# Kernel optimization log

Hardware: AMD Instinct MI355X
Metric: run time of the kernel (lower is better)

The kernel has to match this reference:

```python
import jax, jax.numpy as jnp
import numpy as np

BETA = 0.25  # VQ commitment cost


def setup_inputs() -> dict:
    key = jax.random.key(0)
    ks = jax.random.split(key, 6)
    B, C, H, W = 4096, 10, 32, 32
    Din, D, K = 3 * H * W, 256, 512
    img = jax.random.normal(ks[0], (B, 3, H, W), jnp.float32)
    label = jax.random.randint(ks[1], (B,), 0, C)
    enc_W = jax.random.normal(ks[2], (C, Din, D), jnp.float32) * (1.0 / np.sqrt(Din))
    enc_b = jnp.zeros((C, D), jnp.float32)
    codebook = jax.random.normal(ks[3], (K, D), jnp.float32)
    dec_W = jax.random.normal(ks[4], (D, Din), jnp.float32) * (1.0 / np.sqrt(D))
    dec_b = jnp.zeros((Din,), jnp.float32)
    return {"img": img, "label": label, "enc_W": enc_W, "enc_b": enc_b,
            "codebook": codebook, "dec_W": dec_W, "dec_b": dec_b}


def reference(img, label, enc_W, enc_b, codebook, dec_W, dec_b):
    B = img.shape[0]
    C = enc_W.shape[0]
    x = img.reshape(B, -1)                                   # [B, Din]
    onehot = jax.nn.one_hot(label, C, dtype=x.dtype)         # [B, C]
    # label-routed per-class encoders: encode with every expert, select by label
    z_all = jnp.einsum('bi,cid->bcd', x, enc_W) + enc_b[None]  # [B, C, D]
    z = jnp.einsum('bcd,bc->bd', z_all, onehot)              # [B, D]
    # --- VQ quantizer (shared) ---
    d2 = (jnp.sum(z * z, -1, keepdims=True)
          - 2.0 * (z @ codebook.T)
          + jnp.sum(codebook * codebook, -1)[None])          # [B, K]
    idx = jnp.argmin(d2, axis=-1)                            # [B]
    q = codebook[idx]                                        # [B, D]
    # per-sample VQ loss (mean over latent dim): codebook + beta*commitment
    cb_l = jnp.mean((jax.lax.stop_gradient(z) - q) ** 2, -1)
    cm_l = jnp.mean((z - jax.lax.stop_gradient(q)) ** 2, -1)
    l = cb_l + BETA * cm_l                                   # [B]
    q_st = z + jax.lax.stop_gradient(q - z)                  # straight-through
    # quantization loss = (sum over activated classes of per-subset mean) / n_activated
    counts = jax.ops.segment_sum(jnp.ones((B,), x.dtype), label, num_segments=C)
    sum_l = jax.ops.segment_sum(l, label, num_segments=C)
    present = counts > 0
    per_class = jnp.where(present, sum_l / jnp.maximum(counts, 1.0), 0.0)
    n_act = jnp.maximum(jnp.sum(present.astype(x.dtype)), 1.0)
    quant = jnp.sum(per_class) / n_act
    # shared decoder; scatter-back is identity here since every label has an expert
    dec = q_st @ dec_W + dec_b                               # [B, Din]
    img_out = dec.reshape(img.shape)
    loss = jnp.mean((img_out - img) ** 2) + quant
    return (loss, img_out)
```

## Files before the change

kernel.cpp:

```cpp
#include <hip/hip_runtime.h>
#include <hip/hip_bf16.h>
#include <stddef.h>

#define NB   4096
#define NC   10
#define DIN  3072
#define DD   256
#define KCB  512
#define KSPLIT 8
#define KC   (DIN / KSPLIT)
#define TM   64
#define TGRID 80
#define NIT  (KC / 32)

#define PW_C  786432
#define PW_NH 393216
#define PW_KS 49152
#define PW_IT 4096

typedef unsigned short u16;
typedef short s16x8 __attribute__((ext_vector_type(8)));
typedef float f32x4 __attribute__((ext_vector_type(4)));

__device__ inline void f2bf2(float f, u16& h, u16& l) {
    unsigned uf = __builtin_bit_cast(unsigned, f);
    unsigned uh = (uf + 0x7FFFu + ((uf >> 16) & 1u)) >> 16;
    h = (u16)uh;
    float fh = __builtin_bit_cast(float, uh << 16);
    float r = f - fh;
    unsigned ur = __builtin_bit_cast(unsigned, r);
    l = (u16)((ur + 0x7FFFu + ((ur >> 16) & 1u)) >> 16);
}

__global__ __launch_bounds__(256) void k_wtp(
    const int* __restrict__ label, const float* __restrict__ cb,
    const float* __restrict__ encW, const float* __restrict__ dW,
    int* __restrict__ meta, int* __restrict__ order, float* __restrict__ cbn,
    u16* __restrict__ WtH, u16* __restrict__ WtL,
    u16* __restrict__ dWtH, u16* __restrict__ dWtL, float* __restrict__ cbt)
{
    const int t = threadIdx.x;
    const int bid = blockIdx.x;
    if (bid == 0) {
        __shared__ int cnt_s[NC], cur_s[NC], off_s[NC];
        if (t < NC) { cnt_s[t] = 0; cur_s[t] = 0; }
        __syncthreads();
        for (int b = t; b < NB; b += 256) atomicAdd(&cnt_s[label[b]], 1);
        __syncthreads();
        if (t == 0) {
            int o = 0;
            for (int c = 0; c < NC; ++c) {
                off_s[c] = o; meta[c] = cnt_s[c]; meta[32 + c] = o; o += cnt_s[c];
            }
            meta[32 + NC] = o;
            int ntl = 0;
            for (int c = 0; c < NC; ++c)
                for (int r0 = 0; r0 < cnt_s[c]; r0 += TM) {
                    meta[64 + 2 * ntl] = c; meta[65 + 2 * ntl] = r0; ++ntl;
                }
            meta[63] = ntl;
        }
        __syncthreads();
        for (int b = t; b < NB; b += 256) {
            int c = label[b];
            int p = atomicAdd(&cur_s[c], 1);
            order[off_s[c] + p] = b;
        }
        return;
    }
    if (bid <= 2) {
        int k = (bid - 1) * 256 + t;
        if (k < KCB) {
            const float* r = cb + (size_t)k * DD;
            float a = 0.f;
#pragma unroll 4
            for (int i = 0; i < 64; ++i) {
                float4 v = *(const float4*)(r + i * 4);
                a = fmaf(v.x, v.x, fmaf(v.y, v.y, fmaf(v.z, v.z, fmaf(v.w, v.w, a))));
            }
            cbn[k] = a;
        }
        return;
    }
    const int wb = bid - 3;
    const float* src; int lsrc, ldst, k0, n0;
    u16 *dH = nullptr, *dL = nullptr; float* fdst = nullptr;
    int encw_c = -1;
    if (wb < 1920) {
        int c = wb / 192, rem = wb % 192;
        int kt = rem >> 2, nt = rem & 3;
        k0 = kt * 64; n0 = nt * 64;
        src = encW + (size_t)c * DIN * DD;  lsrc = DD;
        encw_c = c; ldst = 0;
    } else if (wb < 2112) {
        int rem = wb - 1920;
        int kt = rem / 48, nt = rem % 48;
        k0 = kt * 64; n0 = nt * 64;
        src = dW; lsrc = DIN;
        dH = dWtH; dL = dWtL; ldst = DD;
    } else {
        int rem = wb - 2112;
        int kt = rem >> 2, nt = rem & 3;
        k0 = kt * 64; n0 = nt * 64;
        src = cb; lsrc = DD;
        fdst = cbt; ldst = KCB;
    }
    __shared__ float tile[64][65];
    const int trow = t >> 4, tc4 = t & 15;
#pragma unroll
    for (int j = 0; j < 4; ++j) {
        int kk = trow * 4 + j;
        float4 v = *(const float4*)&src[(size_t)(k0 + kk) * lsrc + n0 + tc4 * 4];
        tile[kk][tc4 * 4 + 0] = v.x; tile[kk][tc4 * 4 + 1] = v.y;
        tile[kk][tc4 * 4 + 2] = v.z; tile[kk][tc4 * 4 + 3] = v.w;
    }
    __syncthreads();
    const int n = n0 + (t >> 2), q = t & 3;
    if (fdst) {
#pragma unroll
        for (int j = 0; j < 4; ++j) {
            float4 o = {tile[q * 16 + 4 * j + 0][n - n0], tile[q * 16 + 4 * j + 1][n - n0],
                        tile[q * 16 + 4 * j + 2][n - n0], tile[q * 16 + 4 * j + 3][n - n0]};
            *(float4*)&fdst[(size_t)n * ldst + k0 + q * 16 + 4 * j] = o;
        }
        return;
    }
    s16x8 vh0, vh1, vl0, vl1;
#pragma unroll
    for (int i = 0; i < 8; ++i) {
        u16 h, l;
        f2bf2(tile[q * 16 + i][n - n0], h, l);
        vh0[i] = (short)h; vl0[i] = (short)l;
    }
#pragma unroll
    for (int i = 0; i < 8; ++i) {
        u16 h, l;
        f2bf2(tile[q * 16 + 8 + i][n - n0], h, l);
        vh1[i] = (short)h; vl1[i] = (short)l;
    }
    if (encw_c >= 0) {
        const int nh = n >> 7, cg = (n & 127) >> 4, fr2 = n & 15;
        const size_t nbase = (size_t)encw_c * PW_C + (size_t)nh * PW_NH
                           + (size_t)cg * 512 + (size_t)fr2 * 8;
        int ko = (k0 >> 3) + 2 * q;
        {
            int ks2 = ko / 48, r2 = ko % 48, it2 = r2 >> 2, fg2 = r2 & 3;
            size_t o = nbase + (size_t)ks2 * PW_KS + (size_t)it2 * PW_IT + (size_t)fg2 * 128;
            *(s16x8*)&WtH[o] = vh0; *(s16x8*)&WtL[o] = vl0;
        }
        {
            int ko1 = ko + 1;
            int ks2 = ko1 / 48, r2 = ko1 % 48, it2 = r2 >> 2, fg2 = r2 & 3;
            size_t o = nbase + (size_t)ks2 * PW_KS + (size_t)it2 * PW_IT + (size_t)fg2 * 128;
            *(s16x8*)&WtH[o] = vh1; *(s16x8*)&WtL[o] = vl1;
        }
        return;
    }
    u16* oH = dH + (size_t)n * ldst + k0 + q * 16;
    u16* oL = dL + (size_t)n * ldst + k0 + q * 16;
    *(s16x8*)oH = vh0; *(s16x8*)(oH + 8) = vh1;
    *(s16x8*)oL = vl0; *(s16x8*)(oL + 8) = vl1;
}

__global__ __launch_bounds__(256, 4) void k_enc(
    const float* __restrict__ x, const u16* __restrict__ WpH, const u16* __restrict__ WpL,
    const int* __restrict__ order, const int* __restrict__ meta, float* __restrict__ zpart)
{
    const int bid = blockIdx.x;
    const int sub = bid & 15;
    const int tid = bid >> 4;
    if (tid >= meta[63]) return;
    const int c    = meta[64 + 2 * tid];
    const int row0 = meta[65 + 2 * tid];
    const int ks = sub >> 1, nh = sub & 1;
    const int cnt = meta[c];
    const int off = meta[32 + c];
    const int kbase = ks * KC;

    __shared__ __align__(16) u16 AsH[2048], AsL[2048], BsH[4096], BsL[4096];

    const int t = threadIdx.x;
    const int lane = t & 63;
    const int wid  = t >> 6;
    const int wr = wid >> 1, wc = wid & 1;

    const int ar = ((t >> 6) << 4) | (t & 15);
    const int aq = (t >> 4) & 3;
    int lr = row0 + ar; if (lr > cnt - 1) lr = cnt - 1;
    const float* xp = x + (size_t)order[off + lr] * DIN + kbase + aq * 8;

    const u16* wpH = WpH + (size_t)c * PW_C + (size_t)nh * PW_NH + (size_t)ks * PW_KS + t * 16;
    const u16* wpL = WpL + (size_t)c * PW_C + (size_t)nh * PW_NH + (size_t)ks * PW_KS + t * 16;

    f32x4 acc[2][4];
#pragma unroll
    for (int i = 0; i < 2; ++i)
#pragma unroll
        for (int j = 0; j < 4; ++j) acc[i][j] = (f32x4){0.f, 0.f, 0.f, 0.f};

    const int fr = lane & 15, fg = lane >> 4;
    const int aoffs = t * 8;
    const int boffs = t * 16;
    const int ard0 = ((wr * 2 + 0) * 64 + fg * 16 + fr) * 8;
    const int ard1 = ((wr * 2 + 1) * 64 + fg * 16 + fr) * 8;

    float4 pa0 = *(const float4*)(xp);
    float4 pa1 = *(const float4*)(xp + 4);
    s16x8 ph0 = *(const s16x8*)(wpH);
    s16x8 ph1 = *(const s16x8*)(wpH + 8);
    s16x8 pl0 = *(const s16x8*)(wpL);
    s16x8 pl1 = *(const s16x8*)(wpL + 8);

    for (int it = 0; it < NIT; ++it) {
        {
            float av[8] = {pa0.x, pa0.y, pa0.z, pa0.w, pa1.x, pa1.y, pa1.z, pa1.w};
            s16x8 vh, vl;
#pragma unroll
            for (int i = 0; i < 8; ++i) {
                u16 h, l; f2bf2(av[i], h, l);
                vh[i] = (short)h; vl[i] = (short)l;
            }
            *(s16x8*)&AsH[aoffs] = vh;
            *(s16x8*)&AsL[aoffs] = vl;
            *(s16x8*)&BsH[boffs]     = ph0;
            *(s16x8*)&BsH[boffs + 8] = ph1;
            *(s16x8*)&BsL[boffs]     = pl0;
            *(s16x8*)&BsL[boffs + 8] = pl1;
        }
        __syncthreads();
        if (it + 1 < NIT) {
            const int k0 = (it + 1) * 32;
            const int w0 = (it + 1) * PW_IT;
            pa0 = *(const float4*)(xp + k0);
            pa1 = *(const float4*)(xp + k0 + 4);
            ph0 = *(const s16x8*)(wpH + w0);
            ph1 = *(const s16x8*)(wpH + w0 + 8);
            pl0 = *(const s16x8*)(wpL + w0);
            pl1 = *(const s16x8*)(wpL + w0 + 8);
        }
        s16x8 aH0 = *(const s16x8*)&AsH[ard0];
        s16x8 aH1 = *(const s16x8*)&AsH[ard1];
        s16x8 aL0 = *(const s16x8*)&AsL[ard0];
        s16x8 aL1 = *(const s16x8*)&AsL[ard1];
#pragma unroll
        for (int nt = 0; nt < 4; ++nt) {
            const int brd = ((wc * 4 + nt) * 64 + fg * 16 + fr) * 8;
            s16x8 bH = *(const s16x8*)&BsH[brd];
            s16x8 bL = *(const s16x8*)&BsL[brd];
            acc[0][nt] = __builtin_amdgcn_mfma_f32_16x16x32_bf16(aH0, bH, acc[0][nt], 0, 0, 0);
            acc[0][nt] = __builtin_amdgcn_mfma_f32_16x16x32_bf16(aL0, bH, acc[0][nt], 0, 0, 0);
            acc[0][nt] = __builtin_amdgcn_mfma_f32_16x16x32_bf16(aH0, bL, acc[0][nt], 0, 0, 0);
            acc[1][nt] = __builtin_amdgcn_mfma_f32_16x16x32_bf16(aH1, bH, acc[1][nt], 0, 0, 0);
            acc[1][nt] = __builtin_amdgcn_mfma_f32_16x16x32_bf16(aL1, bH, acc[1][nt], 0, 0, 0);
            acc[1][nt] = __builtin_amdgcn_mfma_f32_16x16x32_bf16(aH1, bL, acc[1][nt], 0, 0, 0);
        }
        __syncthreads();
    }

    float* zp = zpart + (size_t)ks * NB * DD;
#pragma unroll
    for (int mt = 0; mt < 2; ++mt) {
#pragma unroll
        for (int r = 0; r < 4; ++r) {
            int lrow = row0 + wr * 32 + mt * 16 + fg * 4 + r;
            if (lrow < cnt) {
                int gb = order[off + lrow];
                float* dst = zp + (size_t)gb * DD + nh * 128 + wc * 64 + fr;
#pragma unroll
                for (int nt = 0; nt < 4; ++nt)
                    dst[nt * 16] = acc[mt][nt][r];
            }
        }
    }
}

__global__ __launch_bounds__(256, 3) void k_dec(
    const float* __restrict__ cb, const u16* __restrict__ dWtH, const u16* __restrict__ dWtL,
    const float* __restrict__ db, float* __restrict__ dcb)
{
    const int col0 = blockIdx.x * 256;
    const int m0   = blockIdx.y * 64;

    __shared__ u16 AsH[64 * 40], AsL[64 * 40], BsH[256 * 40], BsL[256 * 40];

    const int t = threadIdx.x;
    const int lane = t & 63;
    const int wid  = t >> 6;
    const int wr = wid >> 1, wc = wid & 1;

    const int ar = t >> 2, aq = t & 3;
    const float* ap = cb + (size_t)(m0 + ar) * DD + aq * 8;
    const int bc = t >> 1, bh = t & 1;
    const u16* wH0 = dWtH + (size_t)(col0 + bc) * DD + bh * 16;
    const u16* wH1 = wH0 + (size_t)128 * DD;
    const u16* wL0 = dWtL + (size_t)(col0 + bc) * DD + bh * 16;
    const u16* wL1 = wL0 + (size_t)128 * DD;

    f32x4 acc[2][8];
#pragma unroll
    for (int i = 0; i < 2; ++i)
#pragma unroll
        for (int j = 0; j < 8; ++j) acc[i][j] = (f32x4){0.f, 0.f, 0.f, 0.f};

    const int fr = lane & 15, fg = lane >> 4;
    const int aoff = fg * 8;
    const int awr = ar * 40 + aq * 8;
    const int bw0 = bc * 40 + bh * 16;
    const int bw1 = (bc + 128) * 40 + bh * 16;

    float4 pa0 = *(const float4*)(ap);
    float4 pa1 = *(const float4*)(ap + 4);
    s16x8 ph0 = *(const s16x8*)(wH0);
    s16x8 ph1 = *(const s16x8*)(wH0 + 8);
    s16x8 ph2 = *(const s16x8*)(wH1);
    s16x8 ph3 = *(const s16x8*)(wH1 + 8);
    s16x8 pl0 = *(const s16x8*)(wL0);
    s16x8 pl1 = *(const s16x8*)(wL0 + 8);
    s16x8 pl2 = *(const s16x8*)(wL1);
    s16x8 pl3 = *(const s16x8*)(wL1 + 8);

    for (int it = 0; it < DD / 32; ++it) {
        {
            float av[8] = {pa0.x, pa0.y, pa0.z, pa0.w, pa1.x, pa1.y, pa1.z, pa1.w};
            s16x8 vh, vl;
#pragma unroll
            for (int i = 0; i < 8; ++i) {
                u16 h, l; f2bf2(av[i], h, l);
                vh[i] = (short)h; vl[i] = (short)l;
            }
            *(s16x8*)&AsH[awr] = vh;
            *(s16x8*)&AsL[awr] = vl;
            *(s16x8*)&BsH[bw0]     = ph0;
            *(s16x8*)&BsH[bw0 + 8] = ph1;
            *(s16x8*)&BsH[bw1]     = ph2;
            *(s16x8*)&BsH[bw1 + 8] = ph3;
            *(s16x8*)&BsL[bw0]     = pl0;
            *(s16x8*)&BsL[bw0 + 8] = pl1;
            *(s16x8*)&BsL[bw1]     = pl2;
            *(s16x8*)&BsL[bw1 + 8] = pl3;
        }
        __syncthreads();
        if (it + 1 < DD / 32) {
            const int k0 = (it + 1) * 32;
            pa0 = *(const float4*)(ap + k0);
            pa1 = *(const float4*)(ap + k0 + 4);
            ph0 = *(const s16x8*)(wH0 + k0);
            ph1 = *(const s16x8*)(wH0 + k0 + 8);
            ph2 = *(const s16x8*)(wH1 + k0);
            ph3 = *(const s16x8*)(wH1 + k0 + 8);
            pl0 = *(const s16x8*)(wL0 + k0);
            pl1 = *(const s16x8*)(wL0 + k0 + 8);
            pl2 = *(const s16x8*)(wL1 + k0);
            pl3 = *(const s16x8*)(wL1 + k0 + 8);
        }
        s16x8 aH0 = *(const s16x8*)&AsH[(wr * 32 + fr) * 40 + aoff];
        s16x8 aH1 = *(const s16x8*)&AsH[(wr * 32 + 16 + fr) * 40 + aoff];
        s16x8 aL0 = *(const s16x8*)&AsL[(wr * 32 + fr) * 40 + aoff];
        s16x8 aL1 = *(const s16x8*)&AsL[(wr * 32 + 16 + fr) * 40 + aoff];
#pragma unroll
        for (int nt = 0; nt < 8; ++nt) {
            const int bcol = wc * 128 + nt * 16 + fr;
            s16x8 bH = *(const s16x8*)&BsH[bcol * 40 + aoff];
            s16x8 bL = *(const s16x8*)&BsL[bcol * 40 + aoff];
            acc[0][nt] = __builtin_amdgcn_mfma_f32_16x16x32_bf16(aH0, bH, acc[0][nt], 0, 0, 0);
            acc[0][nt] = __builtin_amdgcn_mfma_f32_16x16x32_bf16(aL0, bH, acc[0][nt], 0, 0, 0);
            acc[0][nt] = __builtin_amdgcn_mfma_f32_16x16x32_bf16(aH0, bL, acc[0][nt], 0, 0, 0);
            acc[1][nt] = __builtin_amdgcn_mfma_f32_16x16x32_bf16(aH1, bH, acc[1][nt], 0, 0, 0);
            acc[1][nt] = __builtin_amdgcn_mfma_f32_16x16x32_bf16(aL1, bH, acc[1][nt], 0, 0, 0);
            acc[1][nt] = __builtin_amdgcn_mfma_f32_16x16x32_bf16(aH1, bL, acc[1][nt], 0, 0, 0);
        }
        __syncthreads();
    }

#pragma unroll
    for (int mt = 0; mt < 2; ++mt) {
#pragma unroll
        for (int r = 0; r < 4; ++r) {
            int grow = m0 + wr * 32 + mt * 16 + fg * 4 + r;
            float* dst = dcb + (size_t)grow * DIN + col0 + wc * 128 + fr;
#pragma unroll
            for (int nt = 0; nt < 8; ++nt)
                dst[nt * 16] = acc[mt][nt][r] + db[col0 + wc * 128 + nt * 16 + fr];
        }
    }
}

__global__ __launch_bounds__(256) void k_zred(
    const float* __restrict__ zpart, const float* __restrict__ encB,
    const int* __restrict__ label, float* __restrict__ z, float* __restrict__ zn)
{
    int id = blockIdx.x * 256 + threadIdx.x;
    int b = id >> 6, c4 = id & 63;
    int lab = label[b];
    float4 s = *(const float4*)&encB[lab * DD + c4 * 4];
    const float* p = zpart + (size_t)b * DD + c4 * 4;
#pragma unroll
    for (int ks = 0; ks < KSPLIT; ++ks) {
        float4 v = *(const float4*)(p + (size_t)ks * NB * DD);
        s.x += v.x; s.y += v.y; s.z += v.z; s.w += v.w;
    }
    *(float4*)&z[(size_t)b * DD + c4 * 4] = s;
    float sq = fmaf(s.x, s.x, fmaf(s.y, s.y, fmaf(s.z, s.z, s.w * s.w)));
#pragma unroll
    for (int o = 32; o > 0; o >>= 1) sq += __shfl_down(sq, o, 64);
    if ((threadIdx.x & 63) == 0) zn[b] = sq;
}

__global__ __launch_bounds__(256) void k_vq(
    const float* __restrict__ z, const float* __restrict__ cbt, const float* __restrict__ cbn,
    float* __restrict__ vmin, int* __restrict__ vidx)
{
    const int sg = blockIdx.x >> 2;
    const int q  = blockIdx.x & 3;
    const int b0 = sg * 32;
    const int code0 = q * 128;

    __shared__ float As[32][36];
    __shared__ float Bs[32][132];

    const int t = threadIdx.x;
    const int tx = t & 31, ty = t >> 5;

    const int ar = t >> 3, akq = t & 7;
    const float* zp = z + (size_t)(b0 + ar) * DD + akq * 4;
    const int bkk = t >> 3, bcq = t & 7;
    const float* cp = cbt + (size_t)bkk * KCB + code0 + bcq * 16;

    float acc[4][4];
#pragma unroll
    for (int i = 0; i < 4; ++i)
#pragma unroll
        for (int j = 0; j < 4; ++j) acc[i][j] = 0.f;

    float4 pa  = *(const float4*)zp;
    float4 pb0 = *(const float4*)(cp);
    float4 pb1 = *(const float4*)(cp + 4);
    float4 pb2 = *(const float4*)(cp + 8);
    float4 pb3 = *(const float4*)(cp + 12);

    for (int it = 0; it < DD / 32; ++it) {
        As[akq * 4 + 0][ar] = pa.x;
        As[akq * 4 + 1][ar] = pa.y;
        As[akq * 4 + 2][ar] = pa.z;
        As[akq * 4 + 3][ar] = pa.w;
        *(float4*)&Bs[bkk][bcq * 16]      = pb0;
        *(float4*)&Bs[bkk][bcq * 16 + 4]  = pb1;
        *(float4*)&Bs[bkk][bcq * 16 + 8]  = pb2;
        *(float4*)&Bs[bkk][bcq * 16 + 12] = pb3;
        __syncthreads();
        if (it + 1 < DD / 32) {
            const float* zpn = zp + (it + 1) * 32;
            const float* cpn = cp + (size_t)(it + 1) * 32 * KCB;
            pa  = *(const float4*)zpn;
            pb0 = *(const float4*)(cpn);
            pb1 = *(const float4*)(cpn + 4);
            pb2 = *(const float4*)(cpn + 8);
            pb3 = *(const float4*)(cpn + 12);
        }
#pragma unroll
        for (int kk = 0; kk < 32; ++kk) {
            float4 a4 = *(const float4*)&As[kk][ty * 4];
            float4 b4 = *(const float4*)&Bs[kk][tx * 4];
            float am[4] = {a4.x, a4.y, a4.z, a4.w};
            float bn[4] = {b4.x, b4.y, b4.z, b4.w};
#pragma unroll
            for (int i = 0; i < 4; ++i)
#pragma unroll
                for (int j = 0; j < 4; ++j)
                    acc[i][j] = fmaf(am[i], bn[j], acc[i][j]);
        }
        __syncthreads();
    }

    float4 cn4 = *(const float4*)&cbn[code0 + tx * 4];
    float cnv[4] = {cn4.x, cn4.y, cn4.z, cn4.w};
#pragma unroll
    for (int i = 0; i < 4; ++i) {
        float m = cnv[0] - 2.f * acc[i][0];
        int bi = code0 + tx * 4;
#pragma unroll
        for (int j = 1; j < 4; ++j) {
            float sc = cnv[j] - 2.f * acc[i][j];
            if (sc < m) { m = sc; bi = code0 + tx * 4 + j; }
        }
#pragma unroll
        for (int mask = 1; mask <= 16; mask <<= 1) {
            float om = __shfl_xor(m, mask, 64);
            int   oi = __shfl_xor(bi, mask, 64);
            bool lowerSelf = (tx & mask) == 0;
            float lm = lowerSelf ? m : om;
            int   li = lowerSelf ? bi : oi;
            float hm = lowerSelf ? om : m;
            int   hi2 = lowerSelf ? oi : bi;
            if (hm < lm) { m = hm; bi = hi2; } else { m = lm; bi = li; }
        }
        if (tx == 0) {
            vmin[(size_t)(b0 + ty * 4 + i) * 4 + q] = m;
            vidx[(size_t)(b0 + ty * 4 + i) * 4 + q] = bi;
        }
    }
}

__global__ __launch_bounds__(256) void k_vqm(
    const float* __restrict__ vmin, const int* __restrict__ vidx, const float* __restrict__ zn,
    int* __restrict__ idxo, float* __restrict__ lo)
{
    int b = blockIdx.x * 256 + threadIdx.x;
    float m = vmin[b * 4]; int bi = vidx[b * 4];
#pragma unroll
    for (int q = 1; q < 4; ++q) {
        float v = vmin[b * 4 + q];
        if (v < m) { m = v; bi = vidx[b * 4 + q]; }
    }
    idxo[b] = bi;
    lo[b] = (zn[b] + m) * (1.25f / 256.f);
}

__global__ __launch_bounds__(256) void k_gather(
    const float* __restrict__ dcb, const int* __restrict__ idxo, const float* __restrict__ img,
    float* __restrict__ out1, float* __restrict__ ssep)
{
    const int b = blockIdx.x;
    const int k = idxo[b];
    const float* src = dcb + (size_t)k * DIN;
    const float* im  = img + (size_t)b * DIN;
    float* o = out1 + (size_t)b * DIN;
    const float4* s4 = (const float4*)src;
    const float4* i4 = (const float4*)im;

    float accv = 0.f;
#pragma unroll
    for (int j = 0; j < 3; ++j) {
        int i = threadIdx.x + j * 256;
        float4 v = s4[i], w = i4[i];
        float dx = v.x - w.x, dy = v.y - w.y, dz = v.z - w.z, dw = v.w - w.w;
        accv = fmaf(dx, dx, fmaf(dy, dy, fmaf(dz, dz, fmaf(dw, dw, accv))));
    }
#pragma unroll
    for (int j = 0; j < 3; ++j) {
        int i = threadIdx.x + j * 256;
        if (i < DIN / 4 - 1) {
            float4 a = s4[i], b2 = s4[i + 1];
            float4 ov = {a.w, b2.x, b2.y, b2.z};
            *(float4*)(o + 3 + 4 * i) = ov;
        }
    }
    if (threadIdx.x == 0) {
        o[0] = src[0]; o[1] = src[1]; o[2] = src[2];
        o[DIN - 1] = src[DIN - 1];
    }

    __shared__ float red[256];
    red[threadIdx.x] = accv;
    __syncthreads();
#pragma unroll
    for (int st = 128; st > 0; st >>= 1) {
        if (threadIdx.x < st) red[threadIdx.x] += red[threadIdx.x + st];
        __syncthreads();
    }
    if (threadIdx.x == 0) ssep[b] = red[0];
}

__global__ __launch_bounds__(256) void k_final(
    const float* __restrict__ ssep, const float* __restrict__ lo, const int* __restrict__ label,
    const int* __restrict__ meta, float* __restrict__ out)
{
    const int t = threadIdx.x;
    __shared__ float red[256];
    __shared__ float csum[NC];

    float se = 0.f;
    for (int b = t; b < NB; b += 256) se += ssep[b];

    float la[NC];
#pragma unroll
    for (int c = 0; c < NC; ++c) la[c] = 0.f;
    for (int b = t; b < NB; b += 256) {
        int c2 = label[b]; float v = lo[b];
#pragma unroll
        for (int cc = 0; cc < NC; ++cc) la[cc] += (cc == c2) ? v : 0.f;
    }

    red[t] = se; __syncthreads();
    for (int st = 128; st > 0; st >>= 1) { if (t < st) red[t] += red[t + st]; __syncthreads(); }
    float sse = red[0];
    __syncthreads();

    for (int cc = 0; cc < NC; ++cc) {
        red[t] = la[cc]; __syncthreads();
        for (int st = 128; st > 0; st >>= 1) { if (t < st) red[t] += red[t + st]; __syncthreads(); }
        if (t == 0) csum[cc] = red[0];
        __syncthreads();
    }

    if (t == 0) {
        float quant = 0.f, nact = 0.f;
        for (int cc = 0; cc < NC; ++cc) {
            int cnt = meta[cc];
            if (cnt > 0) { quant += csum[cc] / (float)cnt; nact += 1.f; }
        }
        if (nact < 1.f) nact = 1.f;
        quant /= nact;
        out[0] = sse / (float)(NB * DIN) + quant;
    }
}

extern "C" void kernel_launch(void* const* d_in, const int* in_sizes, int n_in,
                              void* d_out, int out_size, void* d_ws, size_t ws_size,
                              hipStream_t stream)
{
    const float* img   = (const float*)d_in[0];
    const int*   label = (const int*)d_in[1];
    const float* encW  = (const float*)d_in[2];
    const float* encB  = (const float*)d_in[3];
    const float* cb    = (const float*)d_in[4];
    const float* dW    = (const float*)d_in[5];
    const float* db    = (const float*)d_in[6];
    float* out = (float*)d_out;

    char* w = (char*)d_ws;
    float* zpart = (float*)(w);
    float* dcb   = (float*)(w);
    float* z     = (float*)(w + 33554432);
    u16*   WtH   = (u16*)  (w + 37748736);
    u16*   WtL   = (u16*)  (w + 53477376);
    u16*   dWtH  = (u16*)  (w + 69206016);
    u16*   dWtL  = (u16*)  (w + 70778880);
    float* vmin  = (float*)(w + 72351744);
    int*   vidx  = (int*)  (w + 72417280);
    float* zn    = (float*)(w + 72482816);
    float* lo    = (float*)(w + 72499200);
    float* ssep  = (float*)(w + 72515584);
    int*   idxo  = (int*)  (w + 72531968);
    int*   order = (int*)  (w + 72548352);
    int*   meta  = (int*)  (w + 72564736);
    float* cbn   = (float*)(w + 72568832);
    float* cbt   = (float*)(w + 72570880);

    hipLaunchKernelGGL(k_wtp,    dim3(2147),       dim3(256), 0, stream,
                       label, cb, encW, dW, meta, order, cbn, WtH, WtL, dWtH, dWtL, cbt);
    hipLaunchKernelGGL(k_enc,    dim3(TGRID * 16), dim3(256), 0, stream, img, WtH, WtL, order, meta, zpart);
    hipLaunchKernelGGL(k_zred,   dim3(1024),       dim3(256), 0, stream, zpart, encB, label, z, zn);
    hipLaunchKernelGGL(k_vq,     dim3(512),        dim3(256), 0, stream, z, cbt, cbn, vmin, vidx);
    hipLaunchKernelGGL(k_vqm,    dim3(16),         dim3(256), 0, stream, vmin, vidx, zn, idxo, lo);
    hipLaunchKernelGGL(k_dec,    dim3(12, 8),      dim3(256), 0, stream, cb, dWtH, dWtL, db, dcb);
    hipLaunchKernelGGL(k_gather, dim3(4096),       dim3(256), 0, stream, dcb, idxo, img, out + 1, ssep);
    hipLaunchKernelGGL(k_final,  dim3(1),          dim3(256), 0, stream, ssep, lo, label, meta, out);
}
```

Baseline: 143.8 us.

## Widen encoder tile to full 256 columns with async LDS double-buffered weights

The encoder kernel now computes all 256 output columns per block instead of splitting into two 128-column halves. This halves the number of blocks and doubles reuse of each converted activation tile. Weight tiles are loaded directly into double-buffered shared memory with global_load_lds, so the next tile is prefetched while MFMAs run on the current one. Shared memory use and the accumulator register count grow, and the launch bound drops to 2 blocks per SM, which reduces occupancy.

```diff
diff --git a/kernel.cpp b/kernel.cpp
--- a/kernel.cpp
+++ b/kernel.cpp
@@ -1,6 +1,7 @@
 #include <hip/hip_runtime.h>
 #include <hip/hip_bf16.h>
 #include <stddef.h>
+#include <stdint.h>
 
 #define NB   4096
 #define NC   10
@@ -30,6 +31,13 @@
     float r = f - fh;
     unsigned ur = __builtin_bit_cast(unsigned, r);
     l = (u16)((ur + 0x7FFFu + ((ur >> 16) & 1u)) >> 16);
+}
+
+__device__ __forceinline__ void gl16(const u16* g, u16* l) {
+    __builtin_amdgcn_global_load_lds(
+        (const __attribute__((address_space(1))) unsigned int*)(uintptr_t)g,
+        (__attribute__((address_space(3))) unsigned int*)(unsigned int)(uintptr_t)l,
+        16, 0, 0);
 }
 
 __global__ __launch_bounds__(256) void k_wtp(
@@ -162,113 +170,111 @@
     *(s16x8*)oL = vl0; *(s16x8*)(oL + 8) = vl1;
 }
 
-__global__ __launch_bounds__(256, 4) void k_enc(
+__global__ __launch_bounds__(256, 2) void k_enc(
     const float* __restrict__ x, const u16* __restrict__ WpH, const u16* __restrict__ WpL,
     const int* __restrict__ order, const int* __restrict__ meta, float* __restrict__ zpart)
 {
     const int bid = blockIdx.x;
-    const int sub = bid & 15;
-    const int tid = bid >> 4;
+    const int ks  = bid & 7;
+    const int tid = bid >> 3;
     if (tid >= meta[63]) return;
     const int c    = meta[64 + 2 * tid];
     const int row0 = meta[65 + 2 * tid];
-    const int ks = sub >> 1, nh = sub & 1;
-    const int cnt = meta[c];
-    const int off = meta[32 + c];
+    const int cnt  = meta[c];
+    const int off  = meta[32 + c];
     const int kbase = ks * KC;
 
-    __shared__ __align__(16) u16 AsH[2048], AsL[2048], BsH[4096], BsL[4096];
+    __shared__ __align__(16) u16 AsH[2048], AsL[2048];
+    __shared__ __align__(16) u16 BsH[2][8192], BsL[2][8192];
 
     const int t = threadIdx.x;
     const int lane = t & 63;
-    const int wid  = t >> 6;
-    const int wr = wid >> 1, wc = wid & 1;
+    const int w    = t >> 6;
+    const int fr = lane & 15, fg = lane >> 4;
 
     const int ar = ((t >> 6) << 4) | (t & 15);
     const int aq = (t >> 4) & 3;
     int lr = row0 + ar; if (lr > cnt - 1) lr = cnt - 1;
     const float* xp = x + (size_t)order[off + lr] * DIN + kbase + aq * 8;
-
-    const u16* wpH = WpH + (size_t)c * PW_C + (size_t)nh * PW_NH + (size_t)ks * PW_KS + t * 16;
-    const u16* wpL = WpL + (size_t)c * PW_C + (size_t)nh * PW_NH + (size_t)ks * PW_KS + t * 16;
-
-    f32x4 acc[2][4];
-#pragma unroll
-    for (int i = 0; i < 2; ++i)
+    const int aoffs = t * 8;
+
+    const u16* gchunk = ((w & 2) ? WpL : WpH)
+                      + (size_t)c * PW_C + (size_t)(w & 1) * PW_NH
+                      + (size_t)ks * PW_KS + lane * 8;
+    u16* lchunk = ((w & 2) ? &BsL[0][0] : &BsH[0][0]) + (w & 1) * 4096;
+
+    f32x4 acc[4][4];
+#pragma unroll
+    for (int i = 0; i < 4; ++i)
 #pragma unroll
         for (int j = 0; j < 4; ++j) acc[i][j] = (f32x4){0.f, 0.f, 0.f, 0.f};
 
-    const int fr = lane & 15, fg = lane >> 4;
-    const int aoffs = t * 8;
-    const int boffs = t * 16;
-    const int ard0 = ((wr * 2 + 0) * 64 + fg * 16 + fr) * 8;
-    const int ard1 = ((wr * 2 + 1) * 64 + fg * 16 + fr) * 8;
-
-    float4 pa0 = *(const float4*)(xp);
+    auto cvt_store = [&](float4 a0, float4 a1) {
+        float av[8] = {a0.x, a0.y, a0.z, a0.w, a1.x, a1.y, a1.z, a1.w};
+        s16x8 vh, vl;
+#pragma unroll
+        for (int i = 0; i < 8; ++i) {
+            u16 h, l; f2bf2(av[i], h, l);
+            vh[i] = (short)h; vl[i] = (short)l;
+        }
+        *(s16x8*)&AsH[aoffs] = vh;
+        *(s16x8*)&AsL[aoffs] = vl;
+    };
+
+    float4 pa0 = *(const float4*)xp;
     float4 pa1 = *(const float4*)(xp + 4);
-    s16x8 ph0 = *(const s16x8*)(wpH);
-    s16x8 ph1 = *(const s16x8*)(wpH + 8);
-    s16x8 pl0 = *(const s16x8*)(wpL);
-    s16x8 pl1 = *(const s16x8*)(wpL + 8);
+#pragma unroll
+    for (int i = 0; i < 8; ++i) gl16(gchunk + i * 512, lchunk + i * 512);
+    cvt_store(pa0, pa1);
+
+    const int arb = fg * 128 + fr * 8;
+    const int brb = (w >> 1) * 4096 + (w & 1) * 2048 + arb;
 
     for (int it = 0; it < NIT; ++it) {
-        {
-            float av[8] = {pa0.x, pa0.y, pa0.z, pa0.w, pa1.x, pa1.y, pa1.z, pa1.w};
-            s16x8 vh, vl;
-#pragma unroll
-            for (int i = 0; i < 8; ++i) {
-                u16 h, l; f2bf2(av[i], h, l);
-                vh[i] = (short)h; vl[i] = (short)l;
+        const int pb = it & 1;
+        __syncthreads();
+        if (it + 1 < NIT) {
+            const u16* g = gchunk + (size_t)(it + 1) * PW_IT;
+            u16* l = lchunk + (pb ^ 1) * 8192;
+#pragma unroll
+            for (int i = 0; i < 8; ++i) gl16(g + i * 512, l + i * 512);
+            pa0 = *(const float4*)(xp + (it + 1) * 32);
+            pa1 = *(const float4*)(xp + (it + 1) * 32 + 4);
+        }
+        s16x8 aH[4], aL[4];
+#pragma unroll
+        for (int mt = 0; mt < 4; ++mt) {
+            aH[mt] = *(const s16x8*)&AsH[mt * 512 + arb];
+            aL[mt] = *(const s16x8*)&AsL[mt * 512 + arb];
+        }
+#pragma unroll
+        for (int ct = 0; ct < 4; ++ct) {
+            const int bo = pb * 8192 + ct * 512 + brb;
+            s16x8 bH = *(const s16x8*)&(&BsH[0][0])[bo];
+            s16x8 bL = *(const s16x8*)&(&BsL[0][0])[bo];
+#pragma unroll
+            for (int mt = 0; mt < 4; ++mt) {
+                acc[mt][ct] = __builtin_amdgcn_mfma_f32_16x16x32_bf16(aH[mt], bH, acc[mt][ct], 0, 0, 0);
+                acc[mt][ct] = __builtin_amdgcn_mfma_f32_16x16x32_bf16(aL[mt], bH, acc[mt][ct], 0, 0, 0);
+                acc[mt][ct] = __builtin_amdgcn_mfma_f32_16x16x32_bf16(aH[mt], bL, acc[mt][ct], 0, 0, 0);
             }
-            *(s16x8*)&AsH[aoffs] = vh;
-            *(s16x8*)&AsL[aoffs] = vl;
-            *(s16x8*)&BsH[boffs]     = ph0;
-            *(s16x8*)&BsH[boffs + 8] = ph1;
-            *(s16x8*)&BsL[boffs]     = pl0;
-            *(s16x8*)&BsL[boffs + 8] = pl1;
-        }
-        __syncthreads();
-        if (it + 1 < NIT) {
-            const int k0 = (it + 1) * 32;
-            const int w0 = (it + 1) * PW_IT;
-            pa0 = *(const float4*)(xp + k0);
-            pa1 = *(const float4*)(xp + k0 + 4);
-            ph0 = *(const s16x8*)(wpH + w0);
-            ph1 = *(const s16x8*)(wpH + w0 + 8);
-            pl0 = *(const s16x8*)(wpL + w0);
-            pl1 = *(const s16x8*)(wpL + w0 + 8);
-        }
-        s16x8 aH0 = *(const s16x8*)&AsH[ard0];
-        s16x8 aH1 = *(const s16x8*)&AsH[ard1];
-        s16x8 aL0 = *(const s16x8*)&AsL[ard0];
-        s16x8 aL1 = *(const s16x8*)&AsL[ard1];
-#pragma unroll
-        for (int nt = 0; nt < 4; ++nt) {
-            const int brd = ((wc * 4 + nt) * 64 + fg * 16 + fr) * 8;
-            s16x8 bH = *(const s16x8*)&BsH[brd];
-            s16x8 bL = *(const s16x8*)&BsL[brd];
-            acc[0][nt] = __builtin_amdgcn_mfma_f32_16x16x32_bf16(aH0, bH, acc[0][nt], 0, 0, 0);
-            acc[0][nt] = __builtin_amdgcn_mfma_f32_16x16x32_bf16(aL0, bH, acc[0][nt], 0, 0, 0);
-            acc[0][nt] = __builtin_amdgcn_mfma_f32_16x16x32_bf16(aH0, bL, acc[0][nt], 0, 0, 0);
-            acc[1][nt] = __builtin_amdgcn_mfma_f32_16x16x32_bf16(aH1, bH, acc[1][nt], 0, 0, 0);
-            acc[1][nt] = __builtin_amdgcn_mfma_f32_16x16x32_bf16(aL1, bH, acc[1][nt], 0, 0, 0);
-            acc[1][nt] = __builtin_amdgcn_mfma_f32_16x16x32_bf16(aH1, bL, acc[1][nt], 0, 0, 0);
-        }
-        __syncthreads();
+        }
+        __syncthreads();
+        if (it + 1 < NIT) cvt_store(pa0, pa1);
     }
 
     float* zp = zpart + (size_t)ks * NB * DD;
 #pragma unroll
-    for (int mt = 0; mt < 2; ++mt) {
+    for (int mt = 0; mt < 4; ++mt) {
 #pragma unroll
         for (int r = 0; r < 4; ++r) {
-            int lrow = row0 + wr * 32 + mt * 16 + fg * 4 + r;
+            int lrow = row0 + mt * 16 + fg * 4 + r;
             if (lrow < cnt) {
                 int gb = order[off + lrow];
-                float* dst = zp + (size_t)gb * DD + nh * 128 + wc * 64 + fr;
-#pragma unroll
-                for (int nt = 0; nt < 4; ++nt)
-                    dst[nt * 16] = acc[mt][nt][r];
+                float* dst = zp + (size_t)gb * DD + w * 64 + fr;
+#pragma unroll
+                for (int ct = 0; ct < 4; ++ct)
+                    dst[ct * 16] = acc[mt][ct][r];
             }
         }
     }
@@ -637,13 +643,13 @@
     float* cbn   = (float*)(w + 72568832);
     float* cbt   = (float*)(w + 72570880);
 
-    hipLaunchKernelGGL(k_wtp,    dim3(2147),       dim3(256), 0, stream,
+    hipLaunchKernelGGL(k_wtp,    dim3(2147),      dim3(256), 0, stream,
                        label, cb, encW, dW, meta, order, cbn, WtH, WtL, dWtH, dWtL, cbt);
-    hipLaunchKernelGGL(k_enc,    dim3(TGRID * 16), dim3(256), 0, stream, img, WtH, WtL, order, meta, zpart);
-    hipLaunchKernelGGL(k_zred,   dim3(1024),       dim3(256), 0, stream, zpart, encB, label, z, zn);
-    hipLaunchKernelGGL(k_vq,     dim3(512),        dim3(256), 0, stream, z, cbt, cbn, vmin, vidx);
-    hipLaunchKernelGGL(k_vqm,    dim3(16),         dim3(256), 0, stream, vmin, vidx, zn, idxo, lo);
-    hipLaunchKernelGGL(k_dec,    dim3(12, 8),      dim3(256), 0, stream, cb, dWtH, dWtL, db, dcb);
-    hipLaunchKernelGGL(k_gather, dim3(4096),       dim3(256), 0, stream, dcb, idxo, img, out + 1, ssep);
-    hipLaunchKernelGGL(k_final,  dim3(1),          dim3(256), 0, stream, ssep, lo, label, meta, out);
-}
+    hipLaunchKernelGGL(k_enc,    dim3(TGRID * 8), dim3(256), 0, stream, img, WtH, WtL, order, meta, zpart);
+    hipLaunchKernelGGL(k_zred,   dim3(1024),      dim3(256), 0, stream, zpart, encB, label, z, zn);
+    hipLaunchKernelGGL(k_vq,     dim3(512),       dim3(256), 0, stream, z, cbt, cbn, vmin, vidx);
+    hipLaunchKernelGGL(k_vqm,    dim3(16),        dim3(256), 0, stream, vmin, vidx, zn, idxo, lo);
+    hipLaunchKernelGGL(k_dec,    dim3(12, 8),     dim3(256), 0, stream, cb, dWtH, dWtL, db, dcb);
+    hipLaunchKernelGGL(k_gather, dim3(4096),      dim3(256), 0, stream, dcb, idxo, img, out + 1, ssep);
+    hipLaunchKernelGGL(k_final,  dim3(1),         dim3(256), 0, stream, ssep, lo, label, meta, out);
+}
```

Result: slower. 147.9 us (+2.8%).
